# Performance work log

Hardware: AMD Instinct MI355X
Metric: run time of the kernel (lower is better)

## Reference

```python
import jax, jax.numpy as jnp
import numpy as np

B, S, HID = 1, 2048, 2048
NH, NKV, HD = 32, 8, 64
N_REP = NH // NKV
SCALE = HD ** -0.5
NEG = -1e9  # large negative for causal mask (finite to stay fp16-safe-ish)


def _rope_tables(seq_len, head_dim, base=10000.0):
    inv_freq = 1.0 / (base ** (np.arange(0, head_dim, 2, dtype=np.float32) / head_dim))
    t = np.arange(seq_len, dtype=np.float32)
    freqs = np.outer(t, inv_freq)                      # [S, HD/2]
    emb = np.concatenate([freqs, freqs], axis=-1)      # [S, HD]
    return jnp.asarray(np.cos(emb))[None], jnp.asarray(np.sin(emb))[None]  # [1,S,HD]


def setup_inputs() -> dict:
    key = jax.random.key(0)
    k1, k2, k3, k4, k5 = jax.random.split(key, 5)
    hidden_states = jax.random.normal(k1, (B, S, HID), dtype=jnp.float32)
    cos, sin = _rope_tables(S, HD)
    # causal additive mask [1,1,S,S]
    causal = jnp.tril(jnp.ones((S, S), dtype=bool))
    attention_mask = jnp.where(causal, 0.0, NEG).astype(jnp.float32)[None, None]
    init = 0.02
    wq = jax.random.normal(k2, (NH * HD, HID), dtype=jnp.float32) * init
    wk = jax.random.normal(k3, (NKV * HD, HID), dtype=jnp.float32) * init
    wv = jax.random.normal(k4, (NKV * HD, HID), dtype=jnp.float32) * init
    wo = jax.random.normal(k5, (HID, NH * HD), dtype=jnp.float32) * init
    return {"hidden_states": hidden_states, "cos": cos, "sin": sin,
            "attention_mask": attention_mask, "wq": wq, "wk": wk, "wv": wv, "wo": wo}


def _rotate_half(x):
    x1, x2 = jnp.split(x, 2, axis=-1)
    return jnp.concatenate([-x2, x1], axis=-1)


def reference(hidden_states, cos, sin, attention_mask, wq, wk, wv, wo):
    b, s, _ = hidden_states.shape
    q = (hidden_states @ wq.T).reshape(b, s, NH, HD).transpose(0, 2, 1, 3)   # [b,nh,s,hd]
    k = (hidden_states @ wk.T).reshape(b, s, NKV, HD).transpose(0, 2, 1, 3)  # [b,nkv,s,hd]
    v = (hidden_states @ wv.T).reshape(b, s, NKV, HD).transpose(0, 2, 1, 3)
    c = cos[:, None]  # [b,1,s,hd]
    sn = sin[:, None]
    q = q * c + _rotate_half(q) * sn
    k = k * c + _rotate_half(k) * sn
    # GQA repeat_kv
    k = jnp.repeat(k, N_REP, axis=1)  # [b,nh,s,hd]
    v = jnp.repeat(v, N_REP, axis=1)
    scores = jnp.einsum('bhqd,bhkd->bhqk', q, k) * SCALE
    scores = scores.astype(jnp.float32) + attention_mask
    probs = jax.nn.softmax(scores, axis=-1).astype(q.dtype)  # dropout p=0 (eval)
    attn = jnp.einsum('bhqk,bhkd->bhqd', probs, v)
    attn = attn.transpose(0, 2, 1, 3).reshape(b, s, NH * HD)
    return attn @ wo.T
```

## Files before the change

kernel.cpp:

```cpp
#include <hip/hip_runtime.h>
#include <hip/hip_bf16.h>
#include <stdint.h>


#define S_LEN 2048
#define HIDDEN 2048
#define NH 32
#define NKV 8
#define HD 64
#define SCALE 0.125f

typedef __bf16 bf16x8 __attribute__((ext_vector_type(8)));
typedef float f32x4 __attribute__((ext_vector_type(4)));
typedef float f32x16 __attribute__((ext_vector_type(16)));

__device__ inline void gload16(const void* g, void* l) {
    using GP = const __attribute__((address_space(1))) uint32_t*;
    using LP = __attribute__((address_space(3))) uint32_t*;
    __builtin_amdgcn_global_load_lds((GP)g, (LP)(uint32_t)(uintptr_t)l, 16, 0, 0);
}

__device__ inline ushort bf16r(float x) {
    uint32_t u = __float_as_uint(x);
    return (ushort)((u + 0x7FFFu + ((u >> 16) & 1u)) >> 16);
}
__device__ inline void bsplit(float x, ushort& h, ushort& l) {
    uint32_t u = __float_as_uint(x);
    uint32_t hr = (u + 0x7FFFu + ((u >> 16) & 1u)) >> 16;
    float r = x - __uint_as_float(hr << 16);
    uint32_t ul = __float_as_uint(r);
    l = (ushort)((ul + 0x7FFFu + ((ul >> 16) & 1u)) >> 16);
    h = (ushort)hr;
}

__device__ inline int swz_idx(int row, int fk) {
    int line = row >> 1;
    int inner = (((fk << 1) | (row & 1)) ^ (line & 7));
    return line * 64 + inner * 8;
}

__global__ __launch_bounds__(256) void split_bf16(
    const float* __restrict__ src, ushort* __restrict__ hi,
    ushort* __restrict__ lo, int n4)
{
    int i = blockIdx.x * 256 + threadIdx.x;
    if (i >= n4) return;
    float4 v = ((const float4*)src)[i];
    float x[4] = {v.x, v.y, v.z, v.w};
    ushort h[4], l[4];
#pragma unroll
    for (int j = 0; j < 4; j++) bsplit(x[j], h[j], l[j]);
    ushort4 ho = {h[0], h[1], h[2], h[3]};
    ushort4 lv = {l[0], l[1], l[2], l[3]};
    ((ushort4*)hi)[i] = ho;
    ((ushort4*)lo)[i] = lv;
}

template <int MODE>
__global__ __launch_bounds__(256) void mfma_gemm(
    const ushort* __restrict__ Ah, const ushort* __restrict__ Al,
    const ushort* __restrict__ Bh, const ushort* __restrict__ Bl,
    float* __restrict__ C0, float* __restrict__ C1, float* __restrict__ C2,
    int ldc, int nbx)
{
    __shared__ ushort sAh[64 * 32], sAl[64 * 32];
    __shared__ ushort sBh[128 * 32], sBl[128 * 32];

    const int t = threadIdx.x;
    const int per = (int)gridDim.x >> 3;
    const int id = (blockIdx.x & 7) * per + (blockIdx.x >> 3);
    const int m0 = (id % nbx) * 64;
    const int n0 = (id / nbx) * 128;

    const int lineA = t >> 3;
    const int uA = (t & 7) ^ (lineA & 7);
    const int rowA = lineA * 2 + (uA & 1);
    const int kA = (uA >> 1) * 8;
    const ushort* aH = Ah + (size_t)(m0 + rowA) * HIDDEN + kA;
    const ushort* aL = Al + (size_t)(m0 + rowA) * HIDDEN + kA;
    const ushort* bH0 = Bh + (size_t)(n0 + rowA) * HIDDEN + kA;
    const ushort* bH1 = Bh + (size_t)(n0 + 64 + rowA) * HIDDEN + kA;
    const ushort* bL0 = Bl + (size_t)(n0 + rowA) * HIDDEN + kA;
    const ushort* bL1 = Bl + (size_t)(n0 + 64 + rowA) * HIDDEN + kA;

    const int lane = t & 63, w = t >> 6;
    const int fr = lane & 15;
    const int fk = lane >> 4;

    int idxA[4], idxB[2];
#pragma unroll
    for (int fi = 0; fi < 4; fi++) idxA[fi] = swz_idx(fi * 16 + fr, fk);
#pragma unroll
    for (int fj = 0; fj < 2; fj++) idxB[fj] = swz_idx(w * 32 + fj * 16 + fr, fk);

    f32x4 acc[4][2];
#pragma unroll
    for (int i = 0; i < 4; i++)
#pragma unroll
        for (int j = 0; j < 2; j++) acc[i][j] = {0.f, 0.f, 0.f, 0.f};

    for (int k0 = 0; k0 < HIDDEN; k0 += 32) {
        __syncthreads();
        gload16(aH + k0, sAh + t * 8);
        gload16(aL + k0, sAl + t * 8);
        gload16(bH0 + k0, sBh + t * 8);
        gload16(bH1 + k0, sBh + 2048 + t * 8);
        gload16(bL0 + k0, sBl + t * 8);
        gload16(bL1 + k0, sBl + 2048 + t * 8);
        __syncthreads();

        bf16x8 ah[4], al[4], bh[2], bl[2];
#pragma unroll
        for (int fi = 0; fi < 4; fi++) {
            ah[fi] = *(const bf16x8*)&sAh[idxA[fi]];
            al[fi] = *(const bf16x8*)&sAl[idxA[fi]];
        }
#pragma unroll
        for (int fj = 0; fj < 2; fj++) {
            bh[fj] = *(const bf16x8*)&sBh[idxB[fj]];
            bl[fj] = *(const bf16x8*)&sBl[idxB[fj]];
        }
#pragma unroll
        for (int fi = 0; fi < 4; fi++)
#pragma unroll
            for (int fj = 0; fj < 2; fj++) {
                acc[fi][fj] = __builtin_amdgcn_mfma_f32_16x16x32_bf16(
                    ah[fi], bh[fj], acc[fi][fj], 0, 0, 0);
                acc[fi][fj] = __builtin_amdgcn_mfma_f32_16x16x32_bf16(
                    ah[fi], bl[fj], acc[fi][fj], 0, 0, 0);
                acc[fi][fj] = __builtin_amdgcn_mfma_f32_16x16x32_bf16(
                    al[fi], bh[fj], acc[fi][fj], 0, 0, 0);
            }
    }

#pragma unroll
    for (int fi = 0; fi < 4; fi++)
#pragma unroll
        for (int fj = 0; fj < 2; fj++) {
            int row0 = m0 + fi * 16 + fk * 4;
            int gcol = n0 + w * 32 + fj * 16 + fr;
            if (MODE == 0) {
                int slot = gcol >> 6, cin = gcol & 63;
                float* dst;
                if (slot < NH) dst = C0 + (size_t)slot * S_LEN * HD;
                else if (slot < NH + NKV) dst = C1 + (size_t)(slot - NH) * S_LEN * HD;
                else dst = C2 + (size_t)(slot - NH - NKV) * S_LEN * HD;
#pragma unroll
                for (int i = 0; i < 4; i++)
                    dst[(size_t)(row0 + i) * HD + cin] = acc[fi][fj][i];
            } else {
#pragma unroll
                for (int i = 0; i < 4; i++)
                    C0[(size_t)(row0 + i) * ldc + gcol] = acc[fi][fj][i];
            }
        }
}

__global__ __launch_bounds__(256) void rope_split(
    float* __restrict__ qd, const float* __restrict__ kd,
    const float* __restrict__ cosT, const float* __restrict__ sinT,
    ushort* __restrict__ khi, ushort* __restrict__ klo)
{
    int idx = blockIdx.x * 256 + threadIdx.x;
    int d = idx & 31;
    int s = (idx >> 5) & (S_LEN - 1);
    int slot = idx >> 16;
    float c = cosT[s * HD + d];
    float sn = sinT[s * HD + d];
    if (slot < NH) {
        float* base = qd + ((size_t)slot * S_LEN + s) * HD;
        float x1 = base[d], x2 = base[d + 32];
        base[d] = x1 * c - x2 * sn;
        base[d + 32] = x2 * c + x1 * sn;
    } else {
        const float* base = kd + ((size_t)(slot - NH) * S_LEN + s) * HD;
        float x1 = base[d], x2 = base[d + 32];
        float y1 = x1 * c - x2 * sn;
        float y2 = x2 * c + x1 * sn;
        int sw = (s & 7) << 3;
        size_t rb = ((size_t)(slot - NH) * S_LEN + s) * 64;
        ushort h1, l1, h2, l2;
        bsplit(y1, h1, l1);
        bsplit(y2, h2, l2);
        khi[rb + (d ^ sw)] = h1;        klo[rb + (d ^ sw)] = l1;
        khi[rb + ((d + 32) ^ sw)] = h2; klo[rb + ((d + 32) ^ sw)] = l2;
    }
}

__global__ __launch_bounds__(256) void split_vt(
    const float* __restrict__ v, ushort* __restrict__ vthi,
    ushort* __restrict__ vtlo)
{
    __shared__ float tile[64][65];
    const int b = blockIdx.x;
    const int hk = b >> 5, kt = b & 31;
    const float* src = v + ((size_t)hk * S_LEN + kt * 64) * 64;
    const int t = threadIdx.x;
    {
        int row = t >> 2, dg = (t & 3) * 16;
#pragma unroll
        for (int i = 0; i < 4; i++) {
            float4 x = *(const float4*)(src + row * 64 + dg + i * 4);
            tile[row][dg + i * 4 + 0] = x.x;
            tile[row][dg + i * 4 + 1] = x.y;
            tile[row][dg + i * 4 + 2] = x.z;
            tile[row][dg + i * 4 + 3] = x.w;
        }
    }
    __syncthreads();
    const int d = t >> 2, kg = (t & 3) * 16;
    ushort hi16[16], lo16[16];
#pragma unroll
    for (int i = 0; i < 16; i++) bsplit(tile[kg + i][d], hi16[i], lo16[i]);
    const int sw = (d & 7) << 3;
    size_t rowb = ((size_t)hk * 64 + d) * S_LEN + kt * 64;
    int base = kg ^ (sw & 48);
    int o0 = base + (sw & 8);
    int o1 = base + (8 ^ (sw & 8));
    *(ushort4*)&vthi[rowb + o0]     = *(ushort4*)&hi16[0];
    *(ushort4*)&vthi[rowb + o0 + 4] = *(ushort4*)&hi16[4];
    *(ushort4*)&vthi[rowb + o1]     = *(ushort4*)&hi16[8];
    *(ushort4*)&vthi[rowb + o1 + 4] = *(ushort4*)&hi16[12];
    *(ushort4*)&vtlo[rowb + o0]     = *(ushort4*)&lo16[0];
    *(ushort4*)&vtlo[rowb + o0 + 4] = *(ushort4*)&lo16[4];
    *(ushort4*)&vtlo[rowb + o1]     = *(ushort4*)&lo16[8];
    *(ushort4*)&vtlo[rowb + o1 + 4] = *(ushort4*)&lo16[12];
}

__global__ __launch_bounds__(256) void attn_mfma(
    const float* __restrict__ q,
    const ushort* __restrict__ khi, const ushort* __restrict__ klo,
    const ushort* __restrict__ vthi, const ushort* __restrict__ vtlo,
    ushort* __restrict__ oH, ushort* __restrict__ oL)
{
    __shared__ ushort uni[16384];
    __shared__ ushort Pl[4][32 * 72];
    __shared__ float corrw[4][32];
    __shared__ float lw[4][32];

    const int t = threadIdx.x;
    const int lane = t & 63, w = t >> 6;
    const int hd_ = blockIdx.y, hk = hd_ >> 2;
    const int qt = (int)gridDim.x - 1 - (int)blockIdx.x;
    const int q0 = qt * 128;
    const int l31 = lane & 31;
    const int dh = (lane >> 5) * 8;

    {
        const int row = t >> 1, dg = (t & 1) * 32;
        const float* src = q + ((size_t)hd_ * S_LEN + q0 + row) * HD + dg;
        const int sw = (row & 7) << 3;
#pragma unroll
        for (int i = 0; i < 8; i++) {
            float4 v4 = *(const float4*)(src + i * 4);
            float xs[4] = {v4.x, v4.y, v4.z, v4.w};
            ushort h4[4], l4[4];
#pragma unroll
            for (int j = 0; j < 4; j++) bsplit(xs[j], h4[j], l4[j]);
            int idx = (row * 64 + dg + i * 4) ^ sw;
            *(ushort4*)&uni[idx] = *(ushort4*)&h4[0];
            *(ushort4*)&uni[8192 + idx] = *(ushort4*)&l4[0];
        }
    }
    __syncthreads();
    bf16x8 qh[4], ql[4];
    {
        const int qrow = w * 32 + l31;
        const int sw = (qrow & 7) << 3;
#pragma unroll
        for (int ks = 0; ks < 4; ks++) {
            int idx = (qrow * 64 + ks * 16 + dh) ^ sw;
            qh[ks] = *(const bf16x8*)&uni[idx];
            ql[ks] = *(const bf16x8*)&uni[8192 + idx];
        }
    }

    f32x16 accO0, accO1;
#pragma unroll
    for (int r = 0; r < 16; r++) { accO0[r] = 0.f; accO1[r] = 0.f; }
    float m_run = -1e30f, l_run = 0.f;

    const ushort* khi_t = khi + (size_t)hk * S_LEN * 64;
    const ushort* klo_t = klo + (size_t)hk * S_LEN * 64;
    const ushort* vth_t = vthi + (size_t)hk * 64 * S_LEN;
    const ushort* vtl_t = vtlo + (size_t)hk * 64 * S_LEN;
    ushort* Pw = &Pl[w][0];
    const int swk = (l31 & 7) << 3;
    const int qg = q0 + w * 32 + l31;
    const int d0s = t >> 3, kks = (t & 7) * 8;

    const int ntiles = 2 * qt + 2;
    for (int tile = 0; tile < ntiles; tile++) {
        const int k0 = tile * 64;
        __syncthreads();
        {
            const ushort* a = khi_t + k0 * 64;
            const ushort* b = klo_t + k0 * 64;
            gload16(a + t * 8, &uni[t * 8]);
            gload16(a + 2048 + t * 8, &uni[2048 + t * 8]);
            gload16(b + t * 8, &uni[4096 + t * 8]);
            gload16(b + 2048 + t * 8, &uni[6144 + t * 8]);
            gload16(vth_t + (size_t)d0s * S_LEN + k0 + kks, &uni[8192 + t * 8]);
            gload16(vth_t + (size_t)(d0s + 32) * S_LEN + k0 + kks, &uni[10240 + t * 8]);
            gload16(vtl_t + (size_t)d0s * S_LEN + k0 + kks, &uni[12288 + t * 8]);
            gload16(vtl_t + (size_t)(d0s + 32) * S_LEN + k0 + kks, &uni[14336 + t * 8]);
        }
        __syncthreads();

        f32x16 sc0, sc1;
#pragma unroll
        for (int r = 0; r < 16; r++) { sc0[r] = 0.f; sc1[r] = 0.f; }
#pragma unroll
        for (int ks = 0; ks < 4; ks++) {
            int off = ks * 16 + dh;
            int i0 = (l31 * 64 + off) ^ swk;
            int i1 = ((l31 + 32) * 64 + off) ^ swk;
            bf16x8 kh0 = *(const bf16x8*)&uni[i0];
            bf16x8 kl0 = *(const bf16x8*)&uni[4096 + i0];
            bf16x8 kh1 = *(const bf16x8*)&uni[i1];
            bf16x8 kl1 = *(const bf16x8*)&uni[4096 + i1];
            sc0 = __builtin_amdgcn_mfma_f32_32x32x16_bf16(kh0, qh[ks], sc0, 0, 0, 0);
            sc1 = __builtin_amdgcn_mfma_f32_32x32x16_bf16(kh1, qh[ks], sc1, 0, 0, 0);
            sc0 = __builtin_amdgcn_mfma_f32_32x32x16_bf16(kh0, ql[ks], sc0, 0, 0, 0);
            sc1 = __builtin_amdgcn_mfma_f32_32x32x16_bf16(kh1, ql[ks], sc1, 0, 0, 0);
            sc0 = __builtin_amdgcn_mfma_f32_32x32x16_bf16(kl0, qh[ks], sc0, 0, 0, 0);
            sc1 = __builtin_amdgcn_mfma_f32_32x32x16_bf16(kl1, qh[ks], sc1, 0, 0, 0);
        }

        const bool maskt = (tile >= 2 * qt);
        float mx = -1e30f;
#pragma unroll
        for (int r = 0; r < 16; r++) {
            int krow = (r & 3) + 8 * (r >> 2) + 4 * (lane >> 5);
            float v0 = sc0[r] * SCALE;
            float v1 = sc1[r] * SCALE;
            if (maskt) {
                if (k0 + krow > qg) v0 = -1e30f;
                if (k0 + 32 + krow > qg) v1 = -1e30f;
            }
            sc0[r] = v0; sc1[r] = v1;
            mx = fmaxf(mx, fmaxf(v0, v1));
        }
        mx = fmaxf(mx, __shfl_xor(mx, 32));

        float corr = 1.f;
        const bool skip = __all(mx - m_run <= 8.0f);
        if (!skip) {
            float m_new = fmaxf(m_run, mx);
            corr = __expf(m_run - m_new);
            m_run = m_new;
            if (lane < 32) corrw[w][l31] = corr;
        }
        float sum = 0.f;
#pragma unroll
        for (int r = 0; r < 16; r++) {
            float p0 = __expf(sc0[r] - m_run);
            float p1 = __expf(sc1[r] - m_run);
            sc0[r] = p0; sc1[r] = p1;
            sum += p0 + p1;
        }
        sum += __shfl_xor(sum, 32);
        l_run = l_run * corr + sum;

#pragma unroll
        for (int r = 0; r < 16; r += 2) {
            int krow = (r & 3) + 8 * (r >> 2) + 4 * (lane >> 5);
            uint32_t b0 = (uint32_t)bf16r(sc0[r]) | ((uint32_t)bf16r(sc0[r + 1]) << 16);
            uint32_t b1 = (uint32_t)bf16r(sc1[r]) | ((uint32_t)bf16r(sc1[r + 1]) << 16);
            *(uint32_t*)&Pw[l31 * 72 + krow] = b0;
            *(uint32_t*)&Pw[l31 * 72 + 32 + krow] = b1;
        }

        if (!skip) {
#pragma unroll
            for (int r = 0; r < 16; r++) {
                int qrow = (r & 3) + 8 * (r >> 2) + 4 * (lane >> 5);
                float cr = corrw[w][qrow];
                accO0[r] *= cr; accO1[r] *= cr;
            }
        }

#pragma unroll
        for (int ks = 0; ks < 4; ks++) {
            bf16x8 pa = *(const bf16x8*)&Pw[l31 * 72 + ks * 16 + dh];
            int ia = (l31 * 64 + ks * 16 + dh) ^ swk;
            int ib = ((l31 + 32) * 64 + ks * 16 + dh) ^ swk;
            bf16x8 vh0 = *(const bf16x8*)&uni[8192 + ia];
            bf16x8 vh1 = *(const bf16x8*)&uni[8192 + ib];
            bf16x8 vl0 = *(const bf16x8*)&uni[12288 + ia];
            bf16x8 vl1 = *(const bf16x8*)&uni[12288 + ib];
            accO0 = __builtin_amdgcn_mfma_f32_32x32x16_bf16(pa, vh0, accO0, 0, 0, 0);
            accO1 = __builtin_amdgcn_mfma_f32_32x32x16_bf16(pa, vh1, accO1, 0, 0, 0);
            accO0 = __builtin_amdgcn_mfma_f32_32x32x16_bf16(pa, vl0, accO0, 0, 0, 0);
            accO1 = __builtin_amdgcn_mfma_f32_32x32x16_bf16(pa, vl1, accO1, 0, 0, 0);
        }
    }

    if (lane < 32) lw[w][l31] = l_run;
#pragma unroll
    for (int r = 0; r < 16; r++) {
        int qrow = (r & 3) + 8 * (r >> 2) + 4 * (lane >> 5);
        float inv = 1.0f / lw[w][qrow];
        float v0 = accO0[r] * inv;
        float v1 = accO1[r] * inv;
        size_t base = (size_t)(q0 + w * 32 + qrow) * (NH * HD) + hd_ * 64 + l31;
        ushort hh, ll;
        bsplit(v0, hh, ll);
        oH[base] = hh; oL[base] = ll;
        bsplit(v1, hh, ll);
        oH[base + 32] = hh; oL[base + 32] = ll;
    }
}

extern "C" void kernel_launch(void* const* d_in, const int* in_sizes, int n_in,
                              void* d_out, int out_size, void* d_ws, size_t ws_size,
                              hipStream_t stream) {
    const float* hidden = (const float*)d_in[0];
    const float* cosT   = (const float*)d_in[1];
    const float* sinT   = (const float*)d_in[2];
    const float* wq = (const float*)d_in[4];
    const float* wk = (const float*)d_in[5];
    const float* wv = (const float*)d_in[6];
    const float* wo = (const float*)d_in[7];
    float* out = (float*)d_out;

    char* wsb = (char*)d_ws;
    auto alloc = [&](size_t bytes) { char* p = wsb; wsb += (bytes + 255) & ~255ULL; return p; };
    float* q = (float*)alloc((size_t)NH * S_LEN * HD * 4);
    float* k = (float*)alloc((size_t)NKV * S_LEN * HD * 4);
    float* v = (float*)alloc((size_t)NKV * S_LEN * HD * 4);
    ushort* hidH = (ushort*)alloc((size_t)S_LEN * HIDDEN * 2);
    ushort* hidL = (ushort*)alloc((size_t)S_LEN * HIDDEN * 2);
    ushort* WcH  = (ushort*)alloc((size_t)3072 * HIDDEN * 2);
    ushort* WcL  = (ushort*)alloc((size_t)3072 * HIDDEN * 2);
    ushort* woH  = (ushort*)alloc((size_t)HIDDEN * 2048 * 2);
    ushort* woL  = (ushort*)alloc((size_t)HIDDEN * 2048 * 2);
    ushort* oH   = (ushort*)alloc((size_t)S_LEN * 2048 * 2);
    ushort* oL   = (ushort*)alloc((size_t)S_LEN * 2048 * 2);
    ushort* khi  = hidH;
    ushort* klo  = hidH + 1048576;
    ushort* vthi = hidH + 2097152;
    ushort* vtlo = hidH + 3145728;

    dim3 blk(256);
    {
        int n4 = S_LEN * HIDDEN / 4;
        split_bf16<<<(n4 + 255) / 256, blk, 0, stream>>>(hidden, hidH, hidL, n4);
        int nq4 = NH * HD * HIDDEN / 4;
        split_bf16<<<(nq4 + 255) / 256, blk, 0, stream>>>(wq, WcH, WcL, nq4);
        int nk4 = NKV * HD * HIDDEN / 4;
        size_t off = (size_t)NH * HD * HIDDEN;
        split_bf16<<<(nk4 + 255) / 256, blk, 0, stream>>>(wk, WcH + off, WcL + off, nk4);
        size_t off2 = off + (size_t)NKV * HD * HIDDEN;
        split_bf16<<<(nk4 + 255) / 256, blk, 0, stream>>>(wv, WcH + off2, WcL + off2, nk4);
        int nw4 = HIDDEN * 2048 / 4;
        split_bf16<<<(nw4 + 255) / 256, blk, 0, stream>>>(wo, woH, woL, nw4);
    }
    mfma_gemm<0><<<dim3(32 * 24), blk, 0, stream>>>(
        hidH, hidL, WcH, WcL, q, k, v, 0, 32);
    rope_split<<<(NH + NKV) * S_LEN * 32 / 256, blk, 0, stream>>>(
        q, k, cosT, sinT, khi, klo);
    split_vt<<<NKV * (S_LEN / 64), blk, 0, stream>>>(v, vthi, vtlo);
    attn_mfma<<<dim3(S_LEN / 128, NH), blk, 0, stream>>>(
        q, khi, klo, vthi, vtlo, oH, oL);
    mfma_gemm<1><<<dim3(32 * 16), blk, 0, stream>>>(
        oH, oL, woH, woL, out, nullptr, nullptr, 2048, 32);
}
```

Baseline: 405.3 us.

## Double-buffer attention K/V tiles and build P operands in registers

The attention kernel now prefetches the next K/V tile into a second LDS buffer while computing on the current one, using explicit vmcnt waits and raw barriers. The P matrix is packed in registers with v_permlane32_swap instead of a round trip through LDS. The softmax scale and log2(e) are folded into Q so exp2f can replace __expf. Two other changes add MFMA priority hints and split the QK accumulation into two chains, and the grid is flattened to 1D with head-interleaved scheduling and launch bounds set for 2 blocks per CU. The cost is twice the K/V LDS footprint and reliance on hand-written wait counts.

```diff
diff --git a/kernel.cpp b/kernel.cpp
--- a/kernel.cpp
+++ b/kernel.cpp
@@ -8,7 +8,7 @@
 #define NH 32
 #define NKV 8
 #define HD 64
-#define SCALE 0.125f
+#define SCALE_L2E 0.18033688011112042f
 
 typedef __bf16 bf16x8 __attribute__((ext_vector_type(8)));
 typedef float f32x4 __attribute__((ext_vector_type(4)));
@@ -32,11 +32,8 @@
     l = (ushort)((ul + 0x7FFFu + ((ul >> 16) & 1u)) >> 16);
     h = (ushort)hr;
 }
-
-__device__ inline int swz_idx(int row, int fk) {
-    int line = row >> 1;
-    int inner = (((fk << 1) | (row & 1)) ^ (line & 7));
-    return line * 64 + inner * 8;
+__device__ inline uint32_t pk2(float a, float b) {
+    return (uint32_t)bf16r(a) | ((uint32_t)bf16r(b) << 16);
 }
 
 __global__ __launch_bounds__(256) void split_bf16(
@@ -54,6 +51,12 @@
     ushort4 lv = {l[0], l[1], l[2], l[3]};
     ((ushort4*)hi)[i] = ho;
     ((ushort4*)lo)[i] = lv;
+}
+
+__device__ inline int swz_idx(int row, int fk) {
+    int line = row >> 1;
+    int inner = (((fk << 1) | (row & 1)) ^ (line & 7));
+    return line * 64 + inner * 8;
 }
 
 template <int MODE>
@@ -227,25 +230,55 @@
     *(ushort4*)&vtlo[rowb + o1 + 4] = *(ushort4*)&lo16[12];
 }
 
-__global__ __launch_bounds__(256) void attn_mfma(
+__global__ __launch_bounds__(256, 2) void attn_mfma(
     const float* __restrict__ q,
     const ushort* __restrict__ khi, const ushort* __restrict__ klo,
     const ushort* __restrict__ vthi, const ushort* __restrict__ vtlo,
     ushort* __restrict__ oH, ushort* __restrict__ oL)
 {
-    __shared__ ushort uni[16384];
-    __shared__ ushort Pl[4][32 * 72];
+    __shared__ ushort uni[2][16384];
     __shared__ float corrw[4][32];
     __shared__ float lw[4][32];
 
     const int t = threadIdx.x;
     const int lane = t & 63, w = t >> 6;
-    const int hd_ = blockIdx.y, hk = hd_ >> 2;
-    const int qt = (int)gridDim.x - 1 - (int)blockIdx.x;
+    const int hi = lane >> 5;
+    const int l31 = lane & 31;
+    const int dh = hi * 8;
+
+    const int id = blockIdx.x;
+    const int hd_ = id & 31;
+    const int g = id >> 5;
+    const int qt = (g < 8) ? (15 - g) : (g - 8);
     const int q0 = qt * 128;
-    const int l31 = lane & 31;
-    const int dh = (lane >> 5) * 8;
-
+    const int hk = hd_ >> 2;
+
+    const ushort* khi_t = khi + (size_t)hk * S_LEN * 64;
+    const ushort* klo_t = klo + (size_t)hk * S_LEN * 64;
+    const ushort* vth_t = vthi + (size_t)hk * 64 * S_LEN;
+    const ushort* vtl_t = vtlo + (size_t)hk * 64 * S_LEN;
+    const int d0s = t >> 3, kks = (t & 7) * 8;
+    const int swk = (l31 & 7) << 3;
+    const int qg = q0 + w * 32 + l31;
+    const int ntiles = 2 * qt + 2;
+
+    auto MF = [](bf16x8 a, bf16x8 b, f32x16 c) {
+        return __builtin_amdgcn_mfma_f32_32x32x16_bf16(a, b, c, 0, 0, 0);
+    };
+    auto STAGE = [&](int k0, ushort* buf) {
+        const ushort* a = khi_t + (size_t)k0 * 64;
+        const ushort* b = klo_t + (size_t)k0 * 64;
+        gload16(a + t * 8, buf + t * 8);
+        gload16(a + 2048 + t * 8, buf + 2048 + t * 8);
+        gload16(b + t * 8, buf + 4096 + t * 8);
+        gload16(b + 2048 + t * 8, buf + 6144 + t * 8);
+        gload16(vth_t + (size_t)d0s * S_LEN + k0 + kks, buf + 8192 + t * 8);
+        gload16(vth_t + (size_t)(d0s + 32) * S_LEN + k0 + kks, buf + 10240 + t * 8);
+        gload16(vtl_t + (size_t)d0s * S_LEN + k0 + kks, buf + 12288 + t * 8);
+        gload16(vtl_t + (size_t)(d0s + 32) * S_LEN + k0 + kks, buf + 14336 + t * 8);
+    };
+
+    STAGE(0, uni[0]);
     {
         const int row = t >> 1, dg = (t & 1) * 32;
         const float* src = q + ((size_t)hd_ * S_LEN + q0 + row) * HD + dg;
@@ -256,10 +289,10 @@
             float xs[4] = {v4.x, v4.y, v4.z, v4.w};
             ushort h4[4], l4[4];
 #pragma unroll
-            for (int j = 0; j < 4; j++) bsplit(xs[j], h4[j], l4[j]);
+            for (int j = 0; j < 4; j++) bsplit(xs[j] * SCALE_L2E, h4[j], l4[j]);
             int idx = (row * 64 + dg + i * 4) ^ sw;
-            *(ushort4*)&uni[idx] = *(ushort4*)&h4[0];
-            *(ushort4*)&uni[8192 + idx] = *(ushort4*)&l4[0];
+            *(ushort4*)&uni[1][idx] = *(ushort4*)&h4[0];
+            *(ushort4*)&uni[1][8192 + idx] = *(ushort4*)&l4[0];
         }
     }
     __syncthreads();
@@ -270,136 +303,150 @@
 #pragma unroll
         for (int ks = 0; ks < 4; ks++) {
             int idx = (qrow * 64 + ks * 16 + dh) ^ sw;
-            qh[ks] = *(const bf16x8*)&uni[idx];
-            ql[ks] = *(const bf16x8*)&uni[8192 + idx];
-        }
-    }
+            qh[ks] = *(const bf16x8*)&uni[1][idx];
+            ql[ks] = *(const bf16x8*)&uni[1][8192 + idx];
+        }
+    }
+    __syncthreads();
 
     f32x16 accO0, accO1;
 #pragma unroll
     for (int r = 0; r < 16; r++) { accO0[r] = 0.f; accO1[r] = 0.f; }
     float m_run = -1e30f, l_run = 0.f;
 
-    const ushort* khi_t = khi + (size_t)hk * S_LEN * 64;
-    const ushort* klo_t = klo + (size_t)hk * S_LEN * 64;
-    const ushort* vth_t = vthi + (size_t)hk * 64 * S_LEN;
-    const ushort* vtl_t = vtlo + (size_t)hk * 64 * S_LEN;
-    ushort* Pw = &Pl[w][0];
-    const int swk = (l31 & 7) << 3;
-    const int qg = q0 + w * 32 + l31;
-    const int d0s = t >> 3, kks = (t & 7) * 8;
-
-    const int ntiles = 2 * qt + 2;
     for (int tile = 0; tile < ntiles; tile++) {
         const int k0 = tile * 64;
-        __syncthreads();
-        {
-            const ushort* a = khi_t + k0 * 64;
-            const ushort* b = klo_t + k0 * 64;
-            gload16(a + t * 8, &uni[t * 8]);
-            gload16(a + 2048 + t * 8, &uni[2048 + t * 8]);
-            gload16(b + t * 8, &uni[4096 + t * 8]);
-            gload16(b + 2048 + t * 8, &uni[6144 + t * 8]);
-            gload16(vth_t + (size_t)d0s * S_LEN + k0 + kks, &uni[8192 + t * 8]);
-            gload16(vth_t + (size_t)(d0s + 32) * S_LEN + k0 + kks, &uni[10240 + t * 8]);
-            gload16(vtl_t + (size_t)d0s * S_LEN + k0 + kks, &uni[12288 + t * 8]);
-            gload16(vtl_t + (size_t)(d0s + 32) * S_LEN + k0 + kks, &uni[14336 + t * 8]);
-        }
-        __syncthreads();
-
-        f32x16 sc0, sc1;
-#pragma unroll
-        for (int r = 0; r < 16; r++) { sc0[r] = 0.f; sc1[r] = 0.f; }
-#pragma unroll
-        for (int ks = 0; ks < 4; ks++) {
+        const ushort* U = uni[tile & 1];
+        if (tile + 1 < ntiles) {
+            STAGE(k0 + 64, uni[(tile + 1) & 1]);
+            asm volatile("s_waitcnt vmcnt(8)" ::: "memory");
+        } else {
+            asm volatile("s_waitcnt vmcnt(0)" ::: "memory");
+        }
+        __builtin_amdgcn_s_barrier();
+
+        f32x16 sa0, sa1, sb0, sb1;
+#pragma unroll
+        for (int r = 0; r < 16; r++) { sa0[r] = 0.f; sa1[r] = 0.f; sb0[r] = 0.f; sb1[r] = 0.f; }
+        __builtin_amdgcn_s_setprio(1);
+#pragma unroll
+        for (int ks = 0; ks < 2; ks++) {
             int off = ks * 16 + dh;
             int i0 = (l31 * 64 + off) ^ swk;
             int i1 = ((l31 + 32) * 64 + off) ^ swk;
-            bf16x8 kh0 = *(const bf16x8*)&uni[i0];
-            bf16x8 kl0 = *(const bf16x8*)&uni[4096 + i0];
-            bf16x8 kh1 = *(const bf16x8*)&uni[i1];
-            bf16x8 kl1 = *(const bf16x8*)&uni[4096 + i1];
-            sc0 = __builtin_amdgcn_mfma_f32_32x32x16_bf16(kh0, qh[ks], sc0, 0, 0, 0);
-            sc1 = __builtin_amdgcn_mfma_f32_32x32x16_bf16(kh1, qh[ks], sc1, 0, 0, 0);
-            sc0 = __builtin_amdgcn_mfma_f32_32x32x16_bf16(kh0, ql[ks], sc0, 0, 0, 0);
-            sc1 = __builtin_amdgcn_mfma_f32_32x32x16_bf16(kh1, ql[ks], sc1, 0, 0, 0);
-            sc0 = __builtin_amdgcn_mfma_f32_32x32x16_bf16(kl0, qh[ks], sc0, 0, 0, 0);
-            sc1 = __builtin_amdgcn_mfma_f32_32x32x16_bf16(kl1, qh[ks], sc1, 0, 0, 0);
-        }
-
-        const bool maskt = (tile >= 2 * qt);
+            bf16x8 kh0 = *(const bf16x8*)&U[i0];
+            bf16x8 kl0 = *(const bf16x8*)&U[4096 + i0];
+            bf16x8 kh1 = *(const bf16x8*)&U[i1];
+            bf16x8 kl1 = *(const bf16x8*)&U[4096 + i1];
+            sa0 = MF(kh0, qh[ks], sa0); sa1 = MF(kh1, qh[ks], sa1);
+            sa0 = MF(kh0, ql[ks], sa0); sa1 = MF(kh1, ql[ks], sa1);
+            sa0 = MF(kl0, qh[ks], sa0); sa1 = MF(kl1, qh[ks], sa1);
+        }
+#pragma unroll
+        for (int ks = 2; ks < 4; ks++) {
+            int off = ks * 16 + dh;
+            int i0 = (l31 * 64 + off) ^ swk;
+            int i1 = ((l31 + 32) * 64 + off) ^ swk;
+            bf16x8 kh0 = *(const bf16x8*)&U[i0];
+            bf16x8 kl0 = *(const bf16x8*)&U[4096 + i0];
+            bf16x8 kh1 = *(const bf16x8*)&U[i1];
+            bf16x8 kl1 = *(const bf16x8*)&U[4096 + i1];
+            sb0 = MF(kh0, qh[ks], sb0); sb1 = MF(kh1, qh[ks], sb1);
+            sb0 = MF(kh0, ql[ks], sb0); sb1 = MF(kh1, ql[ks], sb1);
+            sb0 = MF(kl0, qh[ks], sb0); sb1 = MF(kl1, qh[ks], sb1);
+        }
+        __builtin_amdgcn_s_setprio(0);
+        f32x16 sc0 = sa0 + sb0;
+        f32x16 sc1 = sa1 + sb1;
+
+        if (tile >= 2 * qt) {
+#pragma unroll
+            for (int r = 0; r < 16; r++) {
+                int krow = (r & 3) + 8 * (r >> 2) + 4 * hi;
+                if (k0 + krow > qg) sc0[r] = -1e30f;
+                if (k0 + 32 + krow > qg) sc1[r] = -1e30f;
+            }
+        }
         float mx = -1e30f;
 #pragma unroll
-        for (int r = 0; r < 16; r++) {
-            int krow = (r & 3) + 8 * (r >> 2) + 4 * (lane >> 5);
-            float v0 = sc0[r] * SCALE;
-            float v1 = sc1[r] * SCALE;
-            if (maskt) {
-                if (k0 + krow > qg) v0 = -1e30f;
-                if (k0 + 32 + krow > qg) v1 = -1e30f;
-            }
-            sc0[r] = v0; sc1[r] = v1;
-            mx = fmaxf(mx, fmaxf(v0, v1));
-        }
+        for (int r = 0; r < 16; r++) mx = fmaxf(mx, fmaxf(sc0[r], sc1[r]));
         mx = fmaxf(mx, __shfl_xor(mx, 32));
 
+        const bool skip = __all(mx - m_run <= 8.0f);
         float corr = 1.f;
-        const bool skip = __all(mx - m_run <= 8.0f);
         if (!skip) {
             float m_new = fmaxf(m_run, mx);
-            corr = __expf(m_run - m_new);
+            corr = exp2f(m_run - m_new);
             m_run = m_new;
             if (lane < 32) corrw[w][l31] = corr;
         }
         float sum = 0.f;
 #pragma unroll
         for (int r = 0; r < 16; r++) {
-            float p0 = __expf(sc0[r] - m_run);
-            float p1 = __expf(sc1[r] - m_run);
+            float p0 = exp2f(sc0[r] - m_run);
+            float p1 = exp2f(sc1[r] - m_run);
             sc0[r] = p0; sc1[r] = p1;
             sum += p0 + p1;
         }
         sum += __shfl_xor(sum, 32);
         l_run = l_run * corr + sum;
 
-#pragma unroll
-        for (int r = 0; r < 16; r += 2) {
-            int krow = (r & 3) + 8 * (r >> 2) + 4 * (lane >> 5);
-            uint32_t b0 = (uint32_t)bf16r(sc0[r]) | ((uint32_t)bf16r(sc0[r + 1]) << 16);
-            uint32_t b1 = (uint32_t)bf16r(sc1[r]) | ((uint32_t)bf16r(sc1[r + 1]) << 16);
-            *(uint32_t*)&Pw[l31 * 72 + krow] = b0;
-            *(uint32_t*)&Pw[l31 * 72 + 32 + krow] = b1;
+        bf16x8 pa[4];
+        {
+            uint32_t c0, c1, c2, c3;
+            union { uint32_t u[4]; bf16x8 v; } uu;
+#define BUILD_PA(SC, RB, DST)                                              \
+            c0 = pk2((SC)[RB + 0], (SC)[RB + 1]);                          \
+            c1 = pk2((SC)[RB + 2], (SC)[RB + 3]);                          \
+            c2 = pk2((SC)[RB + 4], (SC)[RB + 5]);                          \
+            c3 = pk2((SC)[RB + 6], (SC)[RB + 7]);                          \
+            asm volatile("v_permlane32_swap_b32 %0, %1"                    \
+                         : "+v"(c0), "+v"(c2));                            \
+            asm volatile("v_permlane32_swap_b32 %0, %1"                    \
+                         : "+v"(c1), "+v"(c3));                            \
+            uu.u[0] = c0; uu.u[1] = c1; uu.u[2] = c2; uu.u[3] = c3;        \
+            DST = uu.v;
+            BUILD_PA(sc0, 0, pa[0]);
+            BUILD_PA(sc0, 8, pa[1]);
+            BUILD_PA(sc1, 0, pa[2]);
+            BUILD_PA(sc1, 8, pa[3]);
+#undef BUILD_PA
         }
 
         if (!skip) {
 #pragma unroll
             for (int r = 0; r < 16; r++) {
-                int qrow = (r & 3) + 8 * (r >> 2) + 4 * (lane >> 5);
+                int qrow = (r & 3) + 8 * (r >> 2) + 4 * hi;
                 float cr = corrw[w][qrow];
                 accO0[r] *= cr; accO1[r] *= cr;
             }
         }
 
+        __builtin_amdgcn_s_setprio(1);
 #pragma unroll
         for (int ks = 0; ks < 4; ks++) {
-            bf16x8 pa = *(const bf16x8*)&Pw[l31 * 72 + ks * 16 + dh];
-            int ia = (l31 * 64 + ks * 16 + dh) ^ swk;
-            int ib = ((l31 + 32) * 64 + ks * 16 + dh) ^ swk;
-            bf16x8 vh0 = *(const bf16x8*)&uni[8192 + ia];
-            bf16x8 vh1 = *(const bf16x8*)&uni[8192 + ib];
-            bf16x8 vl0 = *(const bf16x8*)&uni[12288 + ia];
-            bf16x8 vl1 = *(const bf16x8*)&uni[12288 + ib];
-            accO0 = __builtin_amdgcn_mfma_f32_32x32x16_bf16(pa, vh0, accO0, 0, 0, 0);
-            accO1 = __builtin_amdgcn_mfma_f32_32x32x16_bf16(pa, vh1, accO1, 0, 0, 0);
-            accO0 = __builtin_amdgcn_mfma_f32_32x32x16_bf16(pa, vl0, accO0, 0, 0, 0);
-            accO1 = __builtin_amdgcn_mfma_f32_32x32x16_bf16(pa, vl1, accO1, 0, 0, 0);
-        }
+            int off = ks * 16 + dh;
+            int ia = (l31 * 64 + off) ^ swk;
+            int ib = ((l31 + 32) * 64 + off) ^ swk;
+            bf16x8 vh0 = *(const bf16x8*)&U[8192 + ia];
+            bf16x8 vh1 = *(const bf16x8*)&U[8192 + ib];
+            bf16x8 vl0 = *(const bf16x8*)&U[12288 + ia];
+            bf16x8 vl1 = *(const bf16x8*)&U[12288 + ib];
+            accO0 = MF(pa[ks], vh0, accO0);
+            accO1 = MF(pa[ks], vh1, accO1);
+            accO0 = MF(pa[ks], vl0, accO0);
+            accO1 = MF(pa[ks], vl1, accO1);
+        }
+        __builtin_amdgcn_s_setprio(0);
+
+        asm volatile("" ::: "memory");
+        __builtin_amdgcn_s_barrier();
     }
 
     if (lane < 32) lw[w][l31] = l_run;
 #pragma unroll
     for (int r = 0; r < 16; r++) {
-        int qrow = (r & 3) + 8 * (r >> 2) + 4 * (lane >> 5);
+        int qrow = (r & 3) + 8 * (r >> 2) + 4 * hi;
         float inv = 1.0f / lw[w][qrow];
         float v0 = accO0[r] * inv;
         float v1 = accO1[r] * inv;
@@ -461,7 +508,7 @@
     rope_split<<<(NH + NKV) * S_LEN * 32 / 256, blk, 0, stream>>>(
         q, k, cosT, sinT, khi, klo);
     split_vt<<<NKV * (S_LEN / 64), blk, 0, stream>>>(v, vthi, vtlo);
-    attn_mfma<<<dim3(S_LEN / 128, NH), blk, 0, stream>>>(
+    attn_mfma<<<dim3(512), blk, 0, stream>>>(
         q, khi, klo, vthi, vtlo, oH, oL);
     mfma_gemm<1><<<dim3(32 * 16), blk, 0, stream>>>(
         oH, oL, woH, woL, out, nullptr, nullptr, 2048, 32);
```

Measured after the change: 385.9 us. 4.8% less time.
